# Performance work log

Measured on AMD Instinct MI355X. Metric: run time of the kernel, lower is better.

## Reference

```python
import jax, jax.numpy as jnp
import numpy as np

EMBED_DIM = 1024
NUM_HEADS = 16
HEAD_DIM = EMBED_DIM // NUM_HEADS
SCALE = HEAD_DIM ** -0.5


def setup_inputs() -> dict:
    key = jax.random.key(0)
    ks = jax.random.split(key, 5)
    B, N, D = 8, 1024, EMBED_DIM
    std = D ** -0.5
    x = jax.random.normal(ks[0], (B, N, D), dtype=jnp.float32)
    W_qkv = jax.random.normal(ks[1], (D, 3 * D), dtype=jnp.float32) * std
    b_qkv = jnp.zeros((3 * D,), dtype=jnp.float32)
    W_proj = jax.random.normal(ks[2], (D, D), dtype=jnp.float32) * std
    b_proj = jnp.zeros((D,), dtype=jnp.float32)
    return {"x": x, "W_qkv": W_qkv, "b_qkv": b_qkv, "W_proj": W_proj, "b_proj": b_proj}


def reference(x, W_qkv, b_qkv, W_proj, b_proj):
    B, N, D = x.shape
    H, hd = NUM_HEADS, HEAD_DIM
    # QKV projection: (B,N,3D) -> (3,B,H,N,hd)
    qkv = (x @ W_qkv + b_qkv).reshape(B, N, 3, H, hd).transpose(2, 0, 3, 1, 4)
    q, k, v = qkv[0], qkv[1], qkv[2]
    # scaled dot-product attention, full (B,H,N,N) scores as in original
    attn = jnp.einsum('bhqd,bhkd->bhqk', q, k) * SCALE
    attn = jax.nn.softmax(attn, axis=-1)
    out = jnp.einsum('bhqk,bhkd->bhqd', attn, v)  # (B,H,N,hd)
    out = out.transpose(0, 2, 1, 3).reshape(B, N, D)
    return out @ W_proj + b_proj
```

## Files before the change

### kernel.cpp

```cpp
#include <hip/hip_runtime.h>

#define AS1(p) ((const __attribute__((address_space(1))) void*)(p))
#define AS3(p) ((__attribute__((address_space(3))) void*)(p))

typedef __attribute__((ext_vector_type(8))) short bf16x8;
typedef __attribute__((ext_vector_type(4))) float f32x4;
typedef __attribute__((ext_vector_type(16))) float f32x16;

static constexpr int kBatch = 8;
static constexpr int kSeq = 1024;
static constexpr int kD = 1024;
static constexpr int kH = 16;
static constexpr int kHD = 64;
static constexpr int kRows = kBatch * kSeq;
static constexpr int kQKVCols = 3 * kD;

__device__ __forceinline__ unsigned short f2bf(float f) {
  union { float f; unsigned int u; } a; a.f = f;
  unsigned int r = a.u + 0x7fffu + ((a.u >> 16) & 1u);
  return (unsigned short)(r >> 16);
}

__device__ __forceinline__ unsigned pkbf(float a, float b) {
  unsigned r;
  asm("v_cvt_pk_bf16_f32 %0, %1, %2" : "=v"(r) : "v"(a), "v"(b));
  return r;
}

__device__ __forceinline__ float max3f(float a, float b, float c) {
  float r;
  asm("v_max3_f32 %0, %1, %2, %3" : "=v"(r) : "v"(a), "v"(b), "v"(c));
  return r;
}

__device__ __forceinline__ int swap23(int x) {
  return (x & ~12) | ((x & 4) << 1) | ((x & 8) >> 1);
}

__global__ __launch_bounds__(256) void prep_kernel(
    const float* __restrict__ x, unsigned short* __restrict__ Xbf,
    const float* __restrict__ Wqkv, unsigned short* __restrict__ WqkvT,
    const float* __restrict__ Wproj, unsigned short* __restrict__ WpT) {
  const int bid = blockIdx.x, t = threadIdx.x;
  if (bid < 1024) {
    const int n4 = kRows * kD / 4;
    int i = bid * 256 + t;
    const int stride = 1024 * 256;
    for (; i < n4; i += stride) {
      float4 v = reinterpret_cast<const float4*>(x)[i];
      ushort4 o;
      o.x = f2bf(v.x); o.y = f2bf(v.y); o.z = f2bf(v.z); o.w = f2bf(v.w);
      reinterpret_cast<ushort4*>(Xbf)[i] = o;
    }
    return;
  }
  __shared__ float tile[32][33];
  const float* W; unsigned short* Wt; int cols, c0, r0;
  if (bid < 4096) {
    const int idx = bid - 1024;
    W = Wqkv; Wt = WqkvT; cols = kQKVCols;
    c0 = (idx % 96) * 32; r0 = (idx / 96) * 32;
  } else {
    const int idx = bid - 4096;
    W = Wproj; Wt = WpT; cols = kD;
    c0 = (idx % 32) * 32; r0 = (idx / 32) * 32;
  }
  const int tx = t & 31, ty = t >> 5;
#pragma unroll
  for (int i = 0; i < 32; i += 8)
    tile[ty + i][tx] = W[(size_t)(r0 + ty + i) * cols + (c0 + tx)];
  __syncthreads();
#pragma unroll
  for (int i = 0; i < 32; i += 8)
    Wt[(size_t)(c0 + ty + i) * 1024 + (r0 + tx)] = f2bf(tile[tx][ty + i]);
}

__global__ __launch_bounds__(256) void vtrans_kernel(
    const unsigned short* __restrict__ qkv, unsigned short* __restrict__ Vt) {
  __shared__ alignas(16) unsigned short tile[64][72];
  const int nt = blockIdx.x, bh = blockIdx.y;
  const int b = bh >> 4, h = bh & 15;
  const unsigned short* Vb = qkv + (size_t)b * kSeq * kQKVCols + 2 * kD + h * kHD;
  const int t = threadIdx.x;
#pragma unroll
  for (int r = 0; r < 2; ++r) {
    const int c = r * 256 + t;
    const int n = c >> 3, d8 = c & 7;
    uint4 v = *reinterpret_cast<const uint4*>(Vb + (size_t)(nt * 64 + n) * kQKVCols + d8 * 8);
    *reinterpret_cast<uint4*>(&tile[n][d8 * 8]) = v;
  }
  __syncthreads();
#pragma unroll
  for (int r = 0; r < 2; ++r) {
    const int c = r * 256 + t;
    const int d = c >> 3, n8 = c & 7;
    unsigned short w8[8];
#pragma unroll
    for (int j = 0; j < 8; ++j) w8[j] = tile[swap23(n8 * 8 + j)][d];
    *reinterpret_cast<uint4*>(Vt + (size_t)bh * kHD * kSeq + (size_t)d * kSeq + nt * 64 + n8 * 8) =
        *reinterpret_cast<uint4*>(w8);
  }
}

template <int MODE>
__global__ __launch_bounds__(256) void gemm_bt_kernel(
    const unsigned short* __restrict__ A,
    const unsigned short* __restrict__ Bt,
    const float* __restrict__ bias,
    void* __restrict__ Cout, unsigned short* __restrict__ Vt,
    int M, int Nn, int K) {
  constexpr int BK = 64;
  __shared__ alignas(16) unsigned short As[128 * BK];
  __shared__ alignas(16) unsigned short Bs[128 * BK];
  const int t = threadIdx.x;
  const int lane = t & 63;
  const int w = t >> 6;
  const int wr = w >> 1, wc = w & 1;
  const int l15 = lane & 15, lhi = lane >> 4;
  const int nwg = gridDim.x * gridDim.y;
  const int lin = blockIdx.y * gridDim.x + blockIdx.x;
  const int swz = (lin & 7) * (nwg >> 3) + (lin >> 3);
  const int row0 = (swz / gridDim.x) * 128;
  const int col0 = (swz % gridDim.x) * 128;

  f32x4 acc[4][4] = {};
  const int ldsb = (t & ~63) * 16;

  for (int k0 = 0; k0 < K; k0 += BK) {
    __syncthreads();
#pragma unroll
    for (int r = 0; r < 4; ++r) {
      int c = r * 256 + t;
      int arow = c >> 3;
      int ccol = ((c & 7) ^ (arow & 7)) * 8;
      const unsigned short* ga = A + (size_t)(row0 + arow) * K + (k0 + ccol);
      const unsigned short* gb = Bt + (size_t)(col0 + arow) * K + (k0 + ccol);
      char* la = (char*)As + r * 4096 + ldsb;
      char* lb = (char*)Bs + r * 4096 + ldsb;
      __builtin_amdgcn_global_load_lds(AS1(ga), AS3(la), 16, 0, 0);
      __builtin_amdgcn_global_load_lds(AS1(gb), AS3(lb), 16, 0, 0);
    }
    __syncthreads();
#pragma unroll
    for (int kk = 0; kk < 2; ++kk) {
      bf16x8 af[4], bfr[4];
#pragma unroll
      for (int mi = 0; mi < 4; ++mi) {
        int rowa = wr * 64 + mi * 16 + l15;
        int chunk = (kk * 4 + lhi) ^ (rowa & 7);
        af[mi] = *reinterpret_cast<const bf16x8*>((const char*)As + rowa * 128 + chunk * 16);
      }
#pragma unroll
      for (int ni = 0; ni < 4; ++ni) {
        int rowb = wc * 64 + ni * 16 + l15;
        int chunk = (kk * 4 + lhi) ^ (rowb & 7);
        bfr[ni] = *reinterpret_cast<const bf16x8*>((const char*)Bs + rowb * 128 + chunk * 16);
      }
#pragma unroll
      for (int mi = 0; mi < 4; ++mi)
#pragma unroll
        for (int ni = 0; ni < 4; ++ni)
          acc[mi][ni] = __builtin_amdgcn_mfma_f32_16x16x32_bf16(af[mi], bfr[ni], acc[mi][ni], 0, 0, 0);
    }
  }

  if (MODE == 3) {
#pragma unroll
    for (int mi = 0; mi < 4; ++mi) {
      const int rbase = row0 + wr * 64 + mi * 16 + lhi * 4;
      const int b = rbase >> 10, n = rbase & 1023;
      const int nbase = (n & ~63) | swap23(n & 63);
#pragma unroll
      for (int ni = 0; ni < 4; ++ni) {
        const int col = col0 + wc * 64 + ni * 16 + l15;
        const int hv = col >> 6;
        const int d = col & 63;
        const float bv = bias[col];
        uint2 uu;
        uu.x = pkbf(acc[mi][ni][0] + bv, acc[mi][ni][1] + bv);
        uu.y = pkbf(acc[mi][ni][2] + bv, acc[mi][ni][3] + bv);
        *reinterpret_cast<uint2*>(Vt + ((size_t)((b << 4) + hv) << 16) + d * 1024 + nbase) = uu;
      }
    }
    return;
  }

#pragma unroll
  for (int mi = 0; mi < 4; ++mi) {
    int rbase = row0 + wr * 64 + mi * 16 + lhi * 4;
#pragma unroll
    for (int ni = 0; ni < 4; ++ni) {
      int col = col0 + wc * 64 + ni * 16 + l15;
      float bv = bias[col];
#pragma unroll
      for (int j = 0; j < 4; ++j) {
        float v = acc[mi][ni][j] + bv;
        if (MODE != 0)
          ((unsigned short*)Cout)[(size_t)(rbase + j) * Nn + col] = f2bf(v);
        else
          ((float*)Cout)[(size_t)(rbase + j) * Nn + col] = v;
      }
    }
  }
}

#define G256_STAGE_A(BUF, HALF, KT)                                           \
  do {                                                                        \
    char* _d = smem + (BUF) * 65536 + (HALF) * 16384 + ldst;                  \
    const unsigned short* _s0 = Ap + aoff0 + (size_t)(HALF) * halfstep + (KT) * 64; \
    const unsigned short* _s1 = Ap + aoff1 + (size_t)(HALF) * halfstep + (KT) * 64; \
    __builtin_amdgcn_global_load_lds(AS1(_s0), AS3(_d), 16, 0, 0);            \
    __builtin_amdgcn_global_load_lds(AS1(_s1), AS3(_d + 8192), 16, 0, 0);     \
  } while (0)
#define G256_STAGE_B(BUF, HALF, KT)                                           \
  do {                                                                        \
    char* _d = smem + (BUF) * 65536 + 32768 + (HALF) * 16384 + ldst;          \
    const unsigned short* _s0 = Bp + boff0 + (size_t)(HALF) * halfstep + (KT) * 64; \
    const unsigned short* _s1 = Bp + boff1 + (size_t)(HALF) * halfstep + (KT) * 64; \
    __builtin_amdgcn_global_load_lds(AS1(_s0), AS3(_d), 16, 0, 0);            \
    __builtin_amdgcn_global_load_lds(AS1(_s1), AS3(_d + 8192), 16, 0, 0);     \
  } while (0)
#define G256_PHASE(RBUF, QM, QN, STAGE_STMT, DO_VM)                           \
  do {                                                                        \
    const char* _Ab = smem + (RBUF) * 65536 + (QM) * 16384;                   \
    const char* _Bb = smem + (RBUF) * 65536 + 32768 + (QN) * 16384;           \
    bf16x8 _af[2][4], _bf[2][2];                                              \
    _Pragma("unroll") for (int kk = 0; kk < 2; ++kk) {                        \
      _Pragma("unroll") for (int mi = 0; mi < 4; ++mi) {                      \
        const int rr = wm * 64 + mi * 16 + l15;                               \
        const int ch = (kk * 4 + lhi) ^ (rr & 7);                             \
        _af[kk][mi] = *reinterpret_cast<const bf16x8*>(_Ab + rr * 128 + ch * 16); \
      }                                                                       \
      _Pragma("unroll") for (int ni = 0; ni < 2; ++ni) {                      \
        const int rr = wn * 32 + ni * 16 + l15;                               \
        const int ch = (kk * 4 + lhi) ^ (rr & 7);                             \
        _bf[kk][ni] = *reinterpret_cast<const bf16x8*>(_Bb + rr * 128 + ch * 16); \
      }                                                                       \
    }                                                                         \
    STAGE_STMT;                                                               \
    if (DO_VM) asm volatile("s_waitcnt vmcnt(4)" ::: "memory");               \
    asm volatile("" ::: "memory");                                            \
    __builtin_amdgcn_s_barrier();                                             \
    asm volatile("s_waitcnt lgkmcnt(0)" ::: "memory");                        \
    __builtin_amdgcn_sched_barrier(0);                                        \
    __builtin_amdgcn_s_setprio(1);                                            \
    _Pragma("unroll") for (int kk = 0; kk < 2; ++kk)                          \
      _Pragma("unroll") for (int mi = 0; mi < 4; ++mi)                        \
        _Pragma("unroll") for (int ni = 0; ni < 2; ++ni)                      \
          acc[QM][QN][mi][ni] = __builtin_amdgcn_mfma_f32_16x16x32_bf16(      \
              _af[kk][mi], _bf[kk][ni], acc[QM][QN][mi][ni], 0, 0, 0);        \
    __builtin_amdgcn_s_setprio(0);                                            \
    asm volatile("" ::: "memory");                                            \
    __builtin_amdgcn_s_barrier();                                             \
    asm volatile("" ::: "memory");                                            \
  } while (0)

__global__ __launch_bounds__(512, 2) void gemm256_kernel(
    const unsigned short* __restrict__ Ap,
    const unsigned short* __restrict__ Bp,
    const float* __restrict__ bias,
    unsigned short* __restrict__ Cout, int M, int Nn, int K) {
  __shared__ alignas(16) char smem[131072];
  const int t = threadIdx.x;
  const int lane = t & 63;
  const int wid = t >> 6;
  const int wm = wid >> 2, wn = wid & 3;
  const int l15 = lane & 15, lhi = lane >> 4;

  const int nwg = gridDim.x * gridDim.y;
  const int lin = blockIdx.y * gridDim.x + blockIdx.x;
  const int swz = (lin & 7) * (nwg >> 3) + (lin >> 3);
  const int row0 = (swz / gridDim.x) * 256;
  const int col0 = (swz % gridDim.x) * 256;

  const int r0i = t >> 3, r1i = (512 + t) >> 3;
  const int sc0 = ((t & 7) ^ (r0i & 7)) * 8;
  const int sc1 = (((512 + t) & 7) ^ (r1i & 7)) * 8;
  const size_t aoff0 = (size_t)(row0 + r0i) * K + sc0;
  const size_t aoff1 = (size_t)(row0 + r1i) * K + sc1;
  const size_t boff0 = (size_t)(col0 + r0i) * K + sc0;
  const size_t boff1 = (size_t)(col0 + r1i) * K + sc1;
  const size_t halfstep = (size_t)128 * K;
  const int ldst = (t & ~63) * 16;

  f32x4 acc[2][2][4][2] = {};

  G256_STAGE_A(0, 0, 0);
  G256_STAGE_B(0, 1, 0);
  G256_STAGE_A(0, 1, 0);
  G256_STAGE_B(0, 0, 0);
  G256_STAGE_A(1, 0, 1);
  G256_STAGE_B(1, 1, 1);
  asm volatile("s_waitcnt vmcnt(4)" ::: "memory");
  __builtin_amdgcn_s_barrier();
  asm volatile("" ::: "memory");

  const int nkt = K >> 6;
  const int niter = nkt >> 1;
  for (int i = 0; i < niter; ++i) {
    const int tc1 = 2 * i + 1;
    const int tn0 = (2 * i + 2) & (nkt - 1);
    const int tn1 = (2 * i + 3) & (nkt - 1);
    G256_PHASE(0, 0, 0, G256_STAGE_A(1, 1, tc1), 0);
    G256_PHASE(0, 0, 1, G256_STAGE_B(1, 0, tc1), 0);
    G256_PHASE(0, 1, 1, G256_STAGE_A(0, 0, tn0), 0);
    G256_PHASE(0, 1, 0, G256_STAGE_B(0, 1, tn0), 1);
    G256_PHASE(1, 0, 0, G256_STAGE_A(0, 1, tn0), 0);
    G256_PHASE(1, 0, 1, G256_STAGE_B(0, 0, tn0), 0);
    G256_PHASE(1, 1, 1, G256_STAGE_A(1, 0, tn1), 0);
    G256_PHASE(1, 1, 0, G256_STAGE_B(1, 1, tn1), 1);
  }

#pragma unroll
  for (int qm = 0; qm < 2; ++qm)
#pragma unroll
    for (int mi = 0; mi < 4; ++mi) {
      const int rbase = row0 + qm * 128 + wm * 64 + mi * 16 + lhi * 4;
#pragma unroll
      for (int qn = 0; qn < 2; ++qn)
#pragma unroll
        for (int ni = 0; ni < 2; ++ni) {
          const int col = col0 + qn * 128 + wn * 32 + ni * 16 + l15;
          const float bv = bias[col];
#pragma unroll
          for (int j = 0; j < 4; ++j) {
            const float v = acc[qm][qn][mi][ni][j] + bv;
            Cout[(size_t)(rbase + j) * Nn + col] = f2bf(v);
          }
        }
    }
}

__global__ __launch_bounds__(256) void attn_kernel(
    const unsigned short* __restrict__ qkv,
    const unsigned short* __restrict__ Vt,
    unsigned short* __restrict__ ctx) {
  __shared__ alignas(16) char smem[33280];
  const int qt = blockIdx.x >> 7;
  const int bh = blockIdx.x & 127;
  const int b = bh >> 4, h = bh & 15;
  const int t = threadIdx.x, lane = t & 63, w = t >> 6;
  const int l31 = lane & 31, hi = lane >> 5;

  const unsigned short* Qb = qkv + (size_t)b * kSeq * kQKVCols + h * kHD;
  const unsigned short* Kb = Qb + kD;
  const unsigned short* Vtb = Vt + (size_t)bh * kHD * kSeq;

  bf16x8 qf[4];
  const int qrow = qt * 128 + w * 32 + l31;
#pragma unroll
  for (int s = 0; s < 4; ++s)
    qf[s] = *reinterpret_cast<const bf16x8*>(Qb + (size_t)qrow * kQKVCols + s * 16 + hi * 8);

  const int srow = t >> 3;
  const int sc = ((t & 7) ^ (srow & 7)) * 8;
  const unsigned short* gk[2];
  const unsigned short* gv[2];
#pragma unroll
  for (int r = 0; r < 2; ++r) {
    gk[r] = Kb + (size_t)(r * 32 + srow) * kQKVCols + sc;
    gv[r] = Vtb + (size_t)(r * 32 + srow) * kSeq + sc;
  }
  const int wgrp = w * 1040;

  auto stage = [&](int bufb) {
#pragma unroll
    for (int r = 0; r < 2; ++r) {
      char* lk = smem + bufb + r * 4160 + wgrp;
      __builtin_amdgcn_global_load_lds(AS1(gk[r]), AS3(lk), 16, 0, 0);
      __builtin_amdgcn_global_load_lds(AS1(gv[r]), AS3(lk + 8320), 16, 0, 0);
      gk[r] += 64 * kQKVCols;
      gv[r] += 64;
    }
  };

  f32x16 oacc[2] = {};
  float mrun = -3.0e38f, lrun = 0.f;
  constexpr float kSc = 0.125f * 1.44269504f;

  stage(0);
  __syncthreads();
  int cur = 0;
  const int rb7 = l31 & 7, rg = l31 >> 3;
  for (int kt = 0; kt < 16; ++kt) {
    if (kt < 15) stage((cur ^ 1) * 16640);
    const char* Kp = smem + cur * 16640;
    const char* Vp = Kp + 8320;

    f32x16 sacc[2] = {};
    __builtin_amdgcn_s_setprio(1);
#pragma unroll
    for (int nb = 0; nb < 2; ++nb) {
      const char* krow = Kp + (nb * 4 + rg) * 1040 + rb7 * 128;
#pragma unroll
      for (int s = 0; s < 4; ++s) {
        const int ch = (s * 2 + hi) ^ rb7;
        bf16x8 kf = *reinterpret_cast<const bf16x8*>(krow + ch * 16);
        sacc[nb] = __builtin_amdgcn_mfma_f32_32x32x16_bf16(kf, qf[s], sacc[nb], 0, 0, 0);
      }
    }
    __builtin_amdgcn_s_setprio(0);

    float vv[32];
#pragma unroll
    for (int r = 0; r < 16; ++r) { vv[r] = sacc[0][r]; vv[16 + r] = sacc[1][r]; }
    float w1[11];
#pragma unroll
    for (int i = 0; i < 10; ++i) w1[i] = max3f(vv[3 * i], vv[3 * i + 1], vv[3 * i + 2]);
    w1[10] = fmaxf(vv[30], vv[31]);
    const float x0 = max3f(w1[0], w1[1], w1[2]);
    const float x1 = max3f(w1[3], w1[4], w1[5]);
    const float x2 = max3f(w1[6], w1[7], w1[8]);
    const float x3 = fmaxf(w1[9], w1[10]);
    float tm = fmaxf(max3f(x0, x1, x2), x3);
    tm = fmaxf(tm, __shfl_xor(tm, 32, 64));
    const float tms = tm * kSc;
    if (!__all(tms <= mrun + 8.0f)) {
      const float mnew = fmaxf(mrun, tms);
      const float corr = __builtin_amdgcn_exp2f(mrun - mnew);
      mrun = mnew;
      lrun *= corr;
#pragma unroll
      for (int db = 0; db < 2; ++db)
#pragma unroll
        for (int r = 0; r < 16; ++r) oacc[db][r] *= corr;
    }
    float ps0 = 0.f, ps1 = 0.f, ps2 = 0.f, ps3 = 0.f;
#pragma unroll
    for (int nb = 0; nb < 2; ++nb)
#pragma unroll
      for (int r = 0; r < 16; ++r) {
        const float e = __builtin_amdgcn_exp2f(__builtin_fmaf(sacc[nb][r], kSc, -mrun));
        sacc[nb][r] = e;
        if ((r & 3) == 0) ps0 += e;
        else if ((r & 3) == 1) ps1 += e;
        else if ((r & 3) == 2) ps2 += e;
        else ps3 += e;
      }
    float ps = (ps0 + ps1) + (ps2 + ps3);
    lrun += ps + __shfl_xor(ps, 32, 64);

    bf16x8 pf[4];
#pragma unroll
    for (int s = 0; s < 4; ++s) {
      const int nb = s >> 1, h2 = (s & 1) * 8;
      union { unsigned u[4]; bf16x8 v; } pk4;
#pragma unroll
      for (int i = 0; i < 4; ++i)
        pk4.u[i] = pkbf(sacc[nb][h2 + 2 * i], sacc[nb][h2 + 2 * i + 1]);
      pf[s] = pk4.v;
    }

    __builtin_amdgcn_s_setprio(1);
#pragma unroll
    for (int db = 0; db < 2; ++db) {
      const char* vrow = Vp + (db * 4 + rg) * 1040 + rb7 * 128;
#pragma unroll
      for (int s = 0; s < 4; ++s) {
        const int ch = (s * 2 + hi) ^ rb7;
        bf16x8 vf = *reinterpret_cast<const bf16x8*>(vrow + ch * 16);
        oacc[db] = __builtin_amdgcn_mfma_f32_32x32x16_bf16(vf, pf[s], oacc[db], 0, 0, 0);
      }
    }
    __builtin_amdgcn_s_setprio(0);
    __syncthreads();
    cur ^= 1;
  }

  const float rl = 1.0f / lrun;
  const int qlocal = w * 32 + l31;
#pragma unroll
  for (int db = 0; db < 2; ++db)
#pragma unroll
    for (int g = 0; g < 4; ++g) {
      const unsigned u0 = pkbf(oacc[db][g * 4 + 0] * rl, oacc[db][g * 4 + 1] * rl);
      const unsigned u1 = pkbf(oacc[db][g * 4 + 2] * rl, oacc[db][g * 4 + 3] * rl);
      const int ch = db * 4 + g;
      uint2 uu; uu.x = u0; uu.y = u1;
      *reinterpret_cast<uint2*>(smem + qlocal * 128 + ((ch ^ (qlocal & 7)) * 16) + hi * 8) = uu;
    }
  __syncthreads();
#pragma unroll
  for (int it = 0; it < 4; ++it) {
    const int idx = it * 256 + t;
    const int row = idx >> 3, ch = idx & 7;
    const uint4 vv = *reinterpret_cast<const uint4*>(smem + row * 128 + ((ch ^ (row & 7)) * 16));
    *reinterpret_cast<uint4*>(ctx + (size_t)(b * kSeq + qt * 128 + row) * kD + h * kHD + ch * 8) = vv;
  }
}

extern "C" void kernel_launch(void* const* d_in, const int* in_sizes, int n_in,
                              void* d_out, int out_size, void* d_ws, size_t ws_size,
                              hipStream_t stream) {
  const float* x     = (const float*)d_in[0];
  const float* Wqkv  = (const float*)d_in[1];
  const float* bqkv  = (const float*)d_in[2];
  const float* Wproj = (const float*)d_in[3];
  const float* bproj = (const float*)d_in[4];
  float* out = (float*)d_out;

  char* ws = (char*)d_ws;
  size_t oXbf   = 0;
  size_t oWqkvT = oXbf   + (size_t)kRows * kD * 2;
  size_t oWpT   = oWqkvT + (size_t)kQKVCols * kD * 2;
  size_t oQKV   = oWpT   + (size_t)kD * kD * 2;
  size_t oCTX   = oQKV   + (size_t)kRows * kQKVCols * 2;
  size_t oVt    = oCTX   + (size_t)kRows * kD * 2;
  size_t total_base  = oVt;
  size_t total_fused = oVt + (size_t)kRows * kD * 2;
  if (ws_size < total_base) return;
  const bool fused_vt = ws_size >= total_fused;

  unsigned short* Xbf   = (unsigned short*)(ws + oXbf);
  unsigned short* WqkvT = (unsigned short*)(ws + oWqkvT);
  unsigned short* WpT   = (unsigned short*)(ws + oWpT);
  unsigned short* QKV   = (unsigned short*)(ws + oQKV);
  unsigned short* CTX   = (unsigned short*)(ws + oCTX);
  unsigned short* VtF   = (unsigned short*)(ws + oVt);
  unsigned short* VtA   = (unsigned short*)(ws + oXbf);

  prep_kernel<<<5120, 256, 0, stream>>>(x, Xbf, Wqkv, WqkvT, Wproj, WpT);
  if (fused_vt) {
    gemm256_kernel<<<dim3(2048 / 256, kRows / 256), 512, 0, stream>>>(
        Xbf, WqkvT, bqkv, QKV, kRows, kQKVCols, kD);
    gemm_bt_kernel<3><<<dim3(1024 / 128, kRows / 128), 256, 0, stream>>>(
        Xbf, WqkvT + (size_t)2048 * kD, bqkv + 2048, nullptr, VtF,
        kRows, 1024, kD);
    attn_kernel<<<1024, 256, 0, stream>>>(QKV, VtF, CTX);
  } else {
    gemm_bt_kernel<1><<<dim3(kQKVCols / 128, kRows / 128), 256, 0, stream>>>(
        Xbf, WqkvT, bqkv, QKV, nullptr, kRows, kQKVCols, kD);
    vtrans_kernel<<<dim3(16, 128), 256, 0, stream>>>(QKV, VtA);
    attn_kernel<<<1024, 256, 0, stream>>>(QKV, VtA, CTX);
  }
  gemm_bt_kernel<0><<<dim3(kD / 128, kRows / 128), 256, 0, stream>>>(
      CTX, WpT, bproj, out, nullptr, kRows, kD, kD);
}
```

Measured before the change: 156.8 us.

## Triple-buffer K/V tiles in attention and compute row sums with MFMA

Moves the attention kernel's K/V staging from double to triple buffering. It uses explicit vmcnt waits and raw barriers so two tiles stay in flight while one is consumed. It also drops the scalar softmax row-sum accumulation and cross-lane shuffle, and instead computes the denominator with extra MFMAs against a vector of bf16 ones. This adds LDS usage (about 49KB per block), which may reduce occupancy. The row sum is now taken over bf16-rounded probabilities, which slightly changes numerics.

```diff
diff --git a/kernel.cpp b/kernel.cpp
--- a/kernel.cpp
+++ b/kernel.cpp
@@ -335,7 +335,7 @@
     const unsigned short* __restrict__ qkv,
     const unsigned short* __restrict__ Vt,
     unsigned short* __restrict__ ctx) {
-  __shared__ alignas(16) char smem[33280];
+  __shared__ alignas(16) char smem[49920];
   const int qt = blockIdx.x >> 7;
   const int bh = blockIdx.x & 127;
   const int b = bh >> 4, h = bh & 15;
@@ -351,6 +351,10 @@
 #pragma unroll
   for (int s = 0; s < 4; ++s)
     qf[s] = *reinterpret_cast<const bf16x8*>(Qb + (size_t)qrow * kQKVCols + s * 16 + hi * 8);
+
+  bf16x8 ones;
+#pragma unroll
+  for (int i = 0; i < 8; ++i) ones[i] = (short)0x3F80;
 
   const int srow = t >> 3;
   const int sc = ((t & 7) ^ (srow & 7)) * 8;
@@ -375,16 +379,24 @@
   };
 
   f32x16 oacc[2] = {};
-  float mrun = -3.0e38f, lrun = 0.f;
+  f32x16 lacc = {};
+  float mrun = -3.0e38f;
   constexpr float kSc = 0.125f * 1.44269504f;
 
   stage(0);
-  __syncthreads();
-  int cur = 0;
+  stage(16640);
+  asm volatile("s_waitcnt vmcnt(4)" ::: "memory");
+  __builtin_amdgcn_s_barrier();
+  asm volatile("" ::: "memory");
+
+  int roff = 0, woff = 33280;
   const int rb7 = l31 & 7, rg = l31 >> 3;
   for (int kt = 0; kt < 16; ++kt) {
-    if (kt < 15) stage((cur ^ 1) * 16640);
-    const char* Kp = smem + cur * 16640;
+    if (kt < 14) {
+      stage(woff);
+      woff += 16640; if (woff == 49920) woff = 0;
+    }
+    const char* Kp = smem + roff;
     const char* Vp = Kp + 8320;
 
     f32x16 sacc[2] = {};
@@ -419,26 +431,17 @@
       const float mnew = fmaxf(mrun, tms);
       const float corr = __builtin_amdgcn_exp2f(mrun - mnew);
       mrun = mnew;
-      lrun *= corr;
+      lacc[0] *= corr;
 #pragma unroll
       for (int db = 0; db < 2; ++db)
 #pragma unroll
         for (int r = 0; r < 16; ++r) oacc[db][r] *= corr;
     }
-    float ps0 = 0.f, ps1 = 0.f, ps2 = 0.f, ps3 = 0.f;
 #pragma unroll
     for (int nb = 0; nb < 2; ++nb)
 #pragma unroll
-      for (int r = 0; r < 16; ++r) {
-        const float e = __builtin_amdgcn_exp2f(__builtin_fmaf(sacc[nb][r], kSc, -mrun));
-        sacc[nb][r] = e;
-        if ((r & 3) == 0) ps0 += e;
-        else if ((r & 3) == 1) ps1 += e;
-        else if ((r & 3) == 2) ps2 += e;
-        else ps3 += e;
-      }
-    float ps = (ps0 + ps1) + (ps2 + ps3);
-    lrun += ps + __shfl_xor(ps, 32, 64);
+      for (int r = 0; r < 16; ++r)
+        sacc[nb][r] = __builtin_amdgcn_exp2f(__builtin_fmaf(sacc[nb][r], kSc, -mrun));
 
     bf16x8 pf[4];
 #pragma unroll
@@ -462,12 +465,27 @@
         oacc[db] = __builtin_amdgcn_mfma_f32_32x32x16_bf16(vf, pf[s], oacc[db], 0, 0, 0);
       }
     }
+#pragma unroll
+    for (int s = 0; s < 4; ++s)
+      lacc = __builtin_amdgcn_mfma_f32_32x32x16_bf16(ones, pf[s], lacc, 0, 0, 0);
     __builtin_amdgcn_s_setprio(0);
-    __syncthreads();
-    cur ^= 1;
-  }
-
-  const float rl = 1.0f / lrun;
+
+    if (kt < 15) {
+      if (kt == 14)
+        asm volatile("s_waitcnt vmcnt(0) lgkmcnt(0)" ::: "memory");
+      else
+        asm volatile("s_waitcnt vmcnt(4) lgkmcnt(0)" ::: "memory");
+      __builtin_amdgcn_s_barrier();
+      asm volatile("" ::: "memory");
+    }
+    roff += 16640; if (roff == 49920) roff = 0;
+  }
+
+  asm volatile("s_waitcnt vmcnt(0) lgkmcnt(0)" ::: "memory");
+  __builtin_amdgcn_s_barrier();
+  asm volatile("" ::: "memory");
+
+  const float rl = 1.0f / lacc[0];
   const int qlocal = w * 32 + l31;
 #pragma unroll
   for (int db = 0; db < 2; ++db)
```

Result: no change. 158.9 us (+1.4%).

## Use 512-thread attention blocks with 256 query rows and swizzled block order

Applied to the files above, without the earlier changes.

Each attention block now runs 8 waves over 256 query rows, so one K/V tile load in LDS serves twice as many queries. The LDS layout drops the padded 1040-byte row groups in favour of plain 128-byte rows with XOR swizzle, and each thread issues one K and one V global-to-LDS load per stage instead of two each. Block indices are remapped so consecutive blocks spread across heads, which is meant to improve cache locality across the workgroup distribution. In exchange the grid halves to 512 blocks, which may reduce occupancy and latency hiding, and the unpadded layout could bring back LDS bank conflicts.

```diff
diff --git a/kernel.cpp b/kernel.cpp
--- a/kernel.cpp
+++ b/kernel.cpp
@@ -331,13 +331,14 @@
     }
 }
 
-__global__ __launch_bounds__(256) void attn_kernel(
+__global__ __launch_bounds__(512, 4) void attn_kernel(
     const unsigned short* __restrict__ qkv,
     const unsigned short* __restrict__ Vt,
     unsigned short* __restrict__ ctx) {
-  __shared__ alignas(16) char smem[33280];
-  const int qt = blockIdx.x >> 7;
-  const int bh = blockIdx.x & 127;
+  __shared__ alignas(16) char smem[32768];
+  const int lin = blockIdx.x;
+  const int swz = (lin & 7) * 64 + (lin >> 3);
+  const int bh = swz >> 2, qt = swz & 3;
   const int b = bh >> 4, h = bh & 15;
   const int t = threadIdx.x, lane = t & 63, w = t >> 6;
   const int l31 = lane & 31, hi = lane >> 5;
@@ -347,31 +348,22 @@
   const unsigned short* Vtb = Vt + (size_t)bh * kHD * kSeq;
 
   bf16x8 qf[4];
-  const int qrow = qt * 128 + w * 32 + l31;
+  const int qrow = qt * 256 + w * 32 + l31;
 #pragma unroll
   for (int s = 0; s < 4; ++s)
     qf[s] = *reinterpret_cast<const bf16x8*>(Qb + (size_t)qrow * kQKVCols + s * 16 + hi * 8);
 
   const int srow = t >> 3;
   const int sc = ((t & 7) ^ (srow & 7)) * 8;
-  const unsigned short* gk[2];
-  const unsigned short* gv[2];
-#pragma unroll
-  for (int r = 0; r < 2; ++r) {
-    gk[r] = Kb + (size_t)(r * 32 + srow) * kQKVCols + sc;
-    gv[r] = Vtb + (size_t)(r * 32 + srow) * kSeq + sc;
-  }
-  const int wgrp = w * 1040;
+  const unsigned short* gk = Kb + (size_t)srow * kQKVCols + sc;
+  const unsigned short* gv = Vtb + (size_t)srow * kSeq + sc;
+  const int ldst = w * 1024;
 
   auto stage = [&](int bufb) {
-#pragma unroll
-    for (int r = 0; r < 2; ++r) {
-      char* lk = smem + bufb + r * 4160 + wgrp;
-      __builtin_amdgcn_global_load_lds(AS1(gk[r]), AS3(lk), 16, 0, 0);
-      __builtin_amdgcn_global_load_lds(AS1(gv[r]), AS3(lk + 8320), 16, 0, 0);
-      gk[r] += 64 * kQKVCols;
-      gv[r] += 64;
-    }
+    __builtin_amdgcn_global_load_lds(AS1(gk), AS3(smem + bufb + ldst), 16, 0, 0);
+    __builtin_amdgcn_global_load_lds(AS1(gv), AS3(smem + bufb + 8192 + ldst), 16, 0, 0);
+    gk += 64 * kQKVCols;
+    gv += 64;
   };
 
   f32x16 oacc[2] = {};
@@ -381,21 +373,20 @@
   stage(0);
   __syncthreads();
   int cur = 0;
-  const int rb7 = l31 & 7, rg = l31 >> 3;
   for (int kt = 0; kt < 16; ++kt) {
-    if (kt < 15) stage((cur ^ 1) * 16640);
-    const char* Kp = smem + cur * 16640;
-    const char* Vp = Kp + 8320;
+    if (kt < 15) stage((cur ^ 1) * 16384);
+    const char* Kp = smem + cur * 16384;
+    const char* Vp = Kp + 8192;
 
     f32x16 sacc[2] = {};
     __builtin_amdgcn_s_setprio(1);
 #pragma unroll
     for (int nb = 0; nb < 2; ++nb) {
-      const char* krow = Kp + (nb * 4 + rg) * 1040 + rb7 * 128;
+      const int n = nb * 32 + l31;
 #pragma unroll
       for (int s = 0; s < 4; ++s) {
-        const int ch = (s * 2 + hi) ^ rb7;
-        bf16x8 kf = *reinterpret_cast<const bf16x8*>(krow + ch * 16);
+        const int ch = (s * 2 + hi) ^ (n & 7);
+        bf16x8 kf = *reinterpret_cast<const bf16x8*>(Kp + n * 128 + ch * 16);
         sacc[nb] = __builtin_amdgcn_mfma_f32_32x32x16_bf16(kf, qf[s], sacc[nb], 0, 0, 0);
       }
     }
@@ -454,11 +445,11 @@
     __builtin_amdgcn_s_setprio(1);
 #pragma unroll
     for (int db = 0; db < 2; ++db) {
-      const char* vrow = Vp + (db * 4 + rg) * 1040 + rb7 * 128;
+      const int dr = db * 32 + l31;
 #pragma unroll
       for (int s = 0; s < 4; ++s) {
-        const int ch = (s * 2 + hi) ^ rb7;
-        bf16x8 vf = *reinterpret_cast<const bf16x8*>(vrow + ch * 16);
+        const int ch = (s * 2 + hi) ^ (dr & 7);
+        bf16x8 vf = *reinterpret_cast<const bf16x8*>(Vp + dr * 128 + ch * 16);
         oacc[db] = __builtin_amdgcn_mfma_f32_32x32x16_bf16(vf, pf[s], oacc[db], 0, 0, 0);
       }
     }
@@ -482,10 +473,10 @@
   __syncthreads();
 #pragma unroll
   for (int it = 0; it < 4; ++it) {
-    const int idx = it * 256 + t;
+    const int idx = it * 512 + t;
     const int row = idx >> 3, ch = idx & 7;
     const uint4 vv = *reinterpret_cast<const uint4*>(smem + row * 128 + ((ch ^ (row & 7)) * 16));
-    *reinterpret_cast<uint4*>(ctx + (size_t)(b * kSeq + qt * 128 + row) * kD + h * kHD + ch * 8) = vv;
+    *reinterpret_cast<uint4*>(ctx + (size_t)(b * kSeq + qt * 256 + row) * kD + h * kHD + ch * 8) = vv;
   }
 }
 
@@ -526,12 +517,12 @@
     gemm_bt_kernel<3><<<dim3(1024 / 128, kRows / 128), 256, 0, stream>>>(
         Xbf, WqkvT + (size_t)2048 * kD, bqkv + 2048, nullptr, VtF,
         kRows, 1024, kD);
-    attn_kernel<<<1024, 256, 0, stream>>>(QKV, VtF, CTX);
+    attn_kernel<<<512, 512, 0, stream>>>(QKV, VtF, CTX);
   } else {
     gemm_bt_kernel<1><<<dim3(kQKVCols / 128, kRows / 128), 256, 0, stream>>>(
         Xbf, WqkvT, bqkv, QKV, nullptr, kRows, kQKVCols, kD);
     vtrans_kernel<<<dim3(16, 128), 256, 0, stream>>>(QKV, VtA);
-    attn_kernel<<<1024, 256, 0, stream>>>(QKV, VtA, CTX);
+    attn_kernel<<<512, 512, 0, stream>>>(QKV, VtA, CTX);
   }
   gemm_bt_kernel<0><<<dim3(kD / 128, kRows / 128), 256, 0, stream>>>(
       CTX, WpT, bproj, out, nullptr, kRows, kD, kD);
```

Measured after the change: 147.1 us. 6.2% less time.
